# Kernel tuning notes

Hardware: AMD Instinct MI355X
Metric: run time of the kernel (lower is better)

Reference implementation:

```python
import jax, jax.numpy as jnp
import numpy as np

TEMP = 0.07  # softmax temperature T


def _l2norm(x, axis=1, eps=1e-12):
    return x / jnp.clip(jnp.linalg.norm(x, axis=axis, keepdims=True), eps, None)


def setup_inputs() -> dict:
    key = jax.random.key(0)
    k1, k2, k3, k4 = jax.random.split(key, 4)
    B, K, D = 256, 8192, 128
    q = jax.random.normal(k1, (B, D), dtype=jnp.float32)
    ba_queue = _l2norm(jax.random.normal(k2, (K, D), dtype=jnp.float32))
    nonba_queue = _l2norm(jax.random.normal(k3, (K, D), dtype=jnp.float32))
    targets = jax.random.randint(k4, (B,), 0, 2, dtype=jnp.int64)
    return {"q": q, "ba_queue": ba_queue, "nonba_queue": nonba_queue, "targets": targets}


def reference(q, ba_queue, nonba_queue, targets):
    K = ba_queue.shape[0]
    # encoder output is L2-normalized; queues are detached buffers
    qn = _l2norm(q, axis=1)
    all_feature = jnp.concatenate([qn, ba_queue, nonba_queue], axis=0)  # [N, D]
    all_label = jnp.concatenate([
        targets.astype(jnp.int32),
        jnp.ones((K,), dtype=jnp.int32),
        jnp.zeros((K,), dtype=jnp.int32),
    ])  # [N]
    N = all_feature.shape[0]

    # [N, N] similarity logits
    sim = jnp.matmul(all_feature, all_feature.T) / TEMP
    logits = sim - jax.lax.stop_gradient(jnp.max(sim, axis=1, keepdims=True))

    # positive mask (same label), excluding self
    mask = (all_label[:, None] == all_label[None, :]).astype(jnp.float32)
    logits_mask = 1.0 - jnp.eye(N, dtype=jnp.float32)
    mask = mask * logits_mask

    exp_logits = jnp.exp(logits) * logits_mask
    log_prob = logits - jnp.log(jnp.sum(exp_logits, axis=1, keepdims=True))
    mean_log_prob_pos = jnp.sum(mask * log_prob, axis=1) / jnp.sum(mask, axis=1)
    return -jnp.mean(mean_log_prob_pos)
```

## Files before the change

kernel.cpp:

```cpp
#include <hip/hip_runtime.h>
#include <hip/hip_bf16.h>
#include <stdint.h>

#define TEMPERATURE 0.07f
#define SC 20.6099312f

constexpr int NQ = 256;
constexpr int KQ = 8192;
constexpr int D  = 128;
constexpr int N  = NQ + 2 * KQ;
constexpr int CS = 26;
constexpr int CS2 = CS * 2;
constexpr int BN = 128;
constexpr int RBM = N / 128;
constexpr int RBF = N / 256;
constexpr int PB = 520;

typedef float f32x16 __attribute__((ext_vector_type(16)));
typedef int   i32x4  __attribute__((ext_vector_type(4)));
typedef int   i32x8  __attribute__((ext_vector_type(8)));

constexpr size_t OFF_F32  = 0;
constexpr size_t OFF_8    = OFF_F32  + (size_t)NQ * D * 4;
constexpr size_t OFF_8S   = OFF_8    + (size_t)N * D;
constexpr size_t OFF_PART = OFF_8S   + (size_t)N * D;
constexpr size_t OFF_ATOM = OFF_PART + (size_t)CS2 * N * 4;
constexpr size_t ATOM_BYTES = 256 * 8 + 16;

#define MFMA8(a, b, c) __builtin_amdgcn_mfma_scale_f32_32x32x64_f8f6f4( \
    (a), (b), (c), 0, 0, 0, 0x7f7f7f7f, 0, 0x7f7f7f7f)

__global__ __launch_bounds__(256) void k_prep(const float* __restrict__ q,
                                              const float* __restrict__ ba,
                                              const float* __restrict__ nb,
                                              const long long* __restrict__ tgt,
                                              float* __restrict__ ff,
                                              unsigned char* __restrict__ fb8,
                                              unsigned char* __restrict__ fb8s,
                                              unsigned long long* __restrict__ iS) {
    __shared__ float red[4][2][128];
    int wid = threadIdx.x >> 6, lane = threadIdx.x & 63;
    int rbase = blockIdx.x * 32 + wid * 8;
    float s0x = 0.f, s0y = 0.f, s1x = 0.f, s1y = 0.f;
    #pragma unroll
    for (int i = 0; i < 8; ++i) {
        int r = rbase + i;
        const float* src = (r < NQ) ? (q + (size_t)r * D)
                         : (r < NQ + KQ) ? (ba + (size_t)(r - NQ) * D)
                         : (nb + (size_t)(r - NQ - KQ) * D);
        float2 v = *(const float2*)(src + lane * 2);
        float a = v.x, b = v.y;
        int lab;
        if (r < NQ) {
            float ss = a * a + b * b;
            #pragma unroll
            for (int m = 1; m < 64; m <<= 1) ss += __shfl_xor(ss, m);
            float scale = 1.0f / fmaxf(sqrtf(ss), 1e-12f);
            a *= scale; b *= scale;
            lab = (int)tgt[r];
            *(float2*)(ff + (size_t)r * D + lane * 2) = make_float2(a, b);
        } else {
            lab = (r < NQ + KQ) ? 1 : 0;
        }
        int w8  = __builtin_amdgcn_cvt_pk_fp8_f32(a, b, 0, false);
        int w8s = __builtin_amdgcn_cvt_pk_fp8_f32(a * SC, b * SC, 0, false);
        *(unsigned short*)(fb8  + (size_t)r * D + lane * 2) = (unsigned short)w8;
        *(unsigned short*)(fb8s + (size_t)r * D + lane * 2) = (unsigned short)w8s;
        if (lab) { s1x += a; s1y += b; } else { s0x += a; s0y += b; }
    }
    red[wid][0][lane * 2]     = s0x;
    red[wid][0][lane * 2 + 1] = s0y;
    red[wid][1][lane * 2]     = s1x;
    red[wid][1][lane * 2 + 1] = s1y;
    __syncthreads();
    int lab2 = threadIdx.x >> 7, d = threadIdx.x & 127;
    float s = red[0][lab2][d] + red[1][lab2][d] + red[2][lab2][d] + red[3][lab2][d];
    long long fx = __double2ll_rn((double)s * 4294967296.0);
    atomicAdd(&iS[lab2 * 128 + d], (unsigned long long)fx);
}

__global__ __launch_bounds__(256, 4) void k_main(const unsigned char* __restrict__ fb8,
                                                 const unsigned char* __restrict__ fb8s,
                                                 float* __restrict__ part) {
    __shared__ __align__(16) unsigned char lds[2][BN * 128];
    const int bid = blockIdx.x;
    const int rb = bid / CS, cs = bid % CS;
    const int tid = threadIdx.x;
    const int lane = tid & 63;
    const int wid  = tid >> 6;
    const int wr = wid >> 1, wc = wid & 1;
    const int l31 = lane & 31, lhi = lane >> 5;
    const int rw = rb * 128 + wr * 64;

    int soff[4];
    #pragma unroll
    for (int i = 0; i < 4; ++i) {
        int flat = i * 256 + tid;
        int line = flat >> 4, p = flat & 15;
        int pl = p ^ (line & 15);
        soff[i] = (2 * line + (pl >> 3)) * 128 + (pl & 7) * 16;
    }

#define STAGE(T, B) { \
    const unsigned char* base_ = fb8 + ((size_t)(cs + (T) * CS)) * (BN * 128); \
    _Pragma("unroll") \
    for (int i_ = 0; i_ < 4; ++i_) \
        __builtin_amdgcn_global_load_lds( \
            (const __attribute__((address_space(1))) unsigned int*)(base_ + soff[i_]), \
            (__attribute__((address_space(3))) unsigned int*)(&lds[B][(i_ * 256 + tid) * 16]), \
            16, 0, 0); }

#define SYNC() { asm volatile("s_waitcnt vmcnt(0)" ::: "memory"); __builtin_amdgcn_s_barrier(); }

    i32x8 rf[2][2];
    #pragma unroll
    for (int rs = 0; rs < 2; ++rs)
        #pragma unroll
        for (int s = 0; s < 2; ++s)
            rf[rs][s] = *(const i32x8*)(fb8s + (size_t)(rw + rs * 32 + l31) * D + s * 64 + lhi * 32);

    f32x16 z16;
    #pragma unroll
    for (int e = 0; e < 16; ++e) z16[e] = 0.f;

    float2 ps2[2] = {{0.f, 0.f}, {0.f, 0.f}};

    STAGE(0, 0) SYNC()

    #pragma unroll 1
    for (int t = 0; t < 5; ++t) {
        if (t + 1 < 5) STAGE(t + 1, (t & 1) ^ 1)
        const unsigned char* buf = &lds[t & 1][0];

        f32x16 acc[2][2];
        __builtin_amdgcn_s_setprio(1);
        #pragma unroll
        for (int s = 0; s < 2; ++s) {
            #pragma unroll
            for (int cc = 0; cc < 2; ++cc) {
                int crow = wc * 64 + cc * 32 + l31;
                int line = crow >> 1;
                int pb = ((crow & 1) << 3) + s * 4 + lhi * 2;
                const unsigned char* lb = buf + line * 256;
                i32x4 lo = *(const i32x4*)(lb + ((pb    ) ^ (line & 15)) * 16);
                i32x4 hi = *(const i32x4*)(lb + ((pb + 1) ^ (line & 15)) * 16);
                i32x8 a = {lo[0], lo[1], lo[2], lo[3], hi[0], hi[1], hi[2], hi[3]};
                acc[cc][0] = MFMA8(a, rf[0][s], (s == 0) ? z16 : acc[cc][0]);
                acc[cc][1] = MFMA8(a, rf[1][s], (s == 0) ? z16 : acc[cc][1]);
            }
        }
        __builtin_amdgcn_s_setprio(0);

        #pragma unroll
        for (int cc = 0; cc < 2; ++cc)
            #pragma unroll
            for (int rs = 0; rs < 2; ++rs) {
                float2 p = {0.f, 0.f};
                #pragma unroll
                for (int g = 0; g < 8; ++g) {
                    p.x += __builtin_amdgcn_exp2f(acc[cc][rs][2 * g]);
                    p.y += __builtin_amdgcn_exp2f(acc[cc][rs][2 * g + 1]);
                }
                ps2[rs].x += p.x; ps2[rs].y += p.y;
            }

        SYNC()
    }

    float rsum[2] = {ps2[0].x + ps2[0].y, ps2[1].x + ps2[1].y};
    rsum[0] += __shfl_xor(rsum[0], 32);
    rsum[1] += __shfl_xor(rsum[1], 32);
    if (lane < 32) {
        float* dst = part + (size_t)(cs * 2 + wc) * N + rw + lane;
        dst[0]  = rsum[0];
        dst[32] = rsum[1];
    }
#undef STAGE
#undef SYNC
}

__global__ __launch_bounds__(256) void k_rowfin(const float* __restrict__ part,
                                                const float* __restrict__ ff,
                                                const float* __restrict__ ba,
                                                const float* __restrict__ nb,
                                                unsigned long long* __restrict__ atom,
                                                const long long* __restrict__ tgt,
                                                float* __restrict__ out) {
    __shared__ float sS[256];
    __shared__ float red[256];
    __shared__ int scnt[2];
    sS[threadIdx.x] = (float)((double)(long long)atom[threadIdx.x] * (1.0 / 4294967296.0));
    if (threadIdx.x < 64) {
        int c = 0;
        #pragma unroll
        for (int i = 0; i < 4; ++i) c += (int)tgt[threadIdx.x + 64 * i];
        #pragma unroll
        for (int m = 1; m < 64; m <<= 1) c += __shfl_xor(c, m);
        if (threadIdx.x == 0) { scnt[0] = (NQ - c) + KQ; scnt[1] = c + KQ; }
    }
    __syncthreads();
    int r = blockIdx.x * 256 + threadIdx.x;
    float se = 0.f;
    #pragma unroll 4
    for (int c = 0; c < CS2; ++c) se += part[(size_t)c * N + r];
    int lab = (r < NQ) ? (int)tgt[r] : ((r < NQ + KQ) ? 1 : 0);
    const float* fsrc = (r < NQ) ? (ff + (size_t)r * D)
                      : (r < NQ + KQ) ? (ba + (size_t)(r - NQ) * D)
                      : (nb + (size_t)(r - NQ - KQ) * D);
    const float4* frow = (const float4*)fsrc;
    const float4* srow = (const float4*)(sS + lab * 128);
    float dS = 0.f, dd = 0.f;
    #pragma unroll
    for (int i = 0; i < 32; ++i) {
        float4 f = frow[i];
        float4 s = srow[i];
        dS += f.x * s.x + f.y * s.y + f.z * s.z + f.w * s.w;
        int wa  = __builtin_amdgcn_cvt_pk_fp8_f32(f.x, f.y, 0, false);
        int wb  = __builtin_amdgcn_cvt_pk_fp8_f32(f.z, f.w, 0, false);
        int wsa = __builtin_amdgcn_cvt_pk_fp8_f32(f.x * SC, f.y * SC, 0, false);
        int wsb = __builtin_amdgcn_cvt_pk_fp8_f32(f.z * SC, f.w * SC, 0, false);
        dd += __builtin_amdgcn_cvt_f32_fp8(wa, 0) * __builtin_amdgcn_cvt_f32_fp8(wsa, 0)
            + __builtin_amdgcn_cvt_f32_fp8(wa, 1) * __builtin_amdgcn_cvt_f32_fp8(wsa, 1)
            + __builtin_amdgcn_cvt_f32_fp8(wb, 0) * __builtin_amdgcn_cvt_f32_fp8(wsb, 0)
            + __builtin_amdgcn_cvt_f32_fp8(wb, 1) * __builtin_amdgcn_cvt_f32_fp8(wsb, 1);
    }
    se -= __builtin_amdgcn_exp2f(dd);
    float lse = logf(se);
    float P = (float)(scnt[lab] - 1);
    float mlpp = (dS - 1.0f) / (TEMPERATURE * P) - lse;
    red[threadIdx.x] = mlpp;
    __syncthreads();
    for (int s2 = 128; s2 > 0; s2 >>= 1) {
        if (threadIdx.x < s2) red[threadIdx.x] += red[threadIdx.x + s2];
        __syncthreads();
    }
    if (threadIdx.x == 0) {
        unsigned long long* lacc = atom + 256;
        unsigned long long* done = atom + 257;
        long long fx = __double2ll_rn((double)red[0] * 16777216.0);
        atomicAdd(lacc, (unsigned long long)fx);
        __threadfence();
        unsigned long long old = atomicAdd(done, 1ull);
        if (old == (unsigned long long)(RBF - 1)) {
            __threadfence();
            long long tot = (long long)atomicAdd(lacc, 0ull);
            out[0] = (float)(-((double)tot * (1.0 / 16777216.0)) / (double)N);
        }
    }
}

extern "C" void kernel_launch(void* const* d_in, const int* in_sizes, int n_in,
                              void* d_out, int out_size, void* d_ws, size_t ws_size,
                              hipStream_t stream) {
    const float* q       = (const float*)d_in[0];
    const float* ba      = (const float*)d_in[1];
    const float* nb      = (const float*)d_in[2];
    const long long* tgt = (const long long*)d_in[3];
    char* ws = (char*)d_ws;
    float*              ff   = (float*)(ws + OFF_F32);
    unsigned char*      fb8  = (unsigned char*)(ws + OFF_8);
    unsigned char*      fb8s = (unsigned char*)(ws + OFF_8S);
    float*              part = (float*)(ws + OFF_PART);
    unsigned long long* atom = (unsigned long long*)(ws + OFF_ATOM);

    hipMemsetAsync(atom, 0, ATOM_BYTES, stream);
    k_prep  <<<PB,       256, 0, stream>>>(q, ba, nb, tgt, ff, fb8, fb8s, atom);
    k_main  <<<RBM * CS, 256, 0, stream>>>(fb8, fb8s, part);
    k_rowfin<<<RBF,      256, 0, stream>>>(part, ff, ba, nb, atom, tgt, (float*)d_out);
}
```

Baseline: 84.09 us.

## Fuse row finalization into main kernel via last-block-per-row-tile ticket

Removes the separate k_rowfin launch. Each k_main block increments a per-row-block atomic counter, and the last of the CS column-slice blocks for a row tile does the finalization in place: it sums the partials, computes the self term and dot products split across two half-threads per row, then reduces into a global accumulator. This saves a kernel launch and lets finalization overlap with other blocks still doing matmul work. The cost is an extra atomic and fence per block, and finalization now runs on only 128 threads per tile inside a kernel with tight occupancy limits.

```diff
diff --git a/kernel.cpp b/kernel.cpp
--- a/kernel.cpp
+++ b/kernel.cpp
@@ -13,7 +13,6 @@
 constexpr int CS2 = CS * 2;
 constexpr int BN = 128;
 constexpr int RBM = N / 128;
-constexpr int RBF = N / 256;
 constexpr int PB = 520;
 
 typedef float f32x16 __attribute__((ext_vector_type(16)));
@@ -25,7 +24,10 @@
 constexpr size_t OFF_8S   = OFF_8    + (size_t)N * D;
 constexpr size_t OFF_PART = OFF_8S   + (size_t)N * D;
 constexpr size_t OFF_ATOM = OFF_PART + (size_t)CS2 * N * 4;
-constexpr size_t ATOM_BYTES = 256 * 8 + 16;
+constexpr int AT_RBD = 256;
+constexpr int AT_LACC = 390;
+constexpr int AT_DONE2 = 391;
+constexpr size_t ATOM_BYTES = 392 * 8;
 
 #define MFMA8(a, b, c) __builtin_amdgcn_mfma_scale_f32_32x32x64_f8f6f4( \
     (a), (b), (c), 0, 0, 0, 0x7f7f7f7f, 0, 0x7f7f7f7f)
@@ -81,8 +83,15 @@
 
 __global__ __launch_bounds__(256, 4) void k_main(const unsigned char* __restrict__ fb8,
                                                  const unsigned char* __restrict__ fb8s,
-                                                 float* __restrict__ part) {
+                                                 const float* __restrict__ ff,
+                                                 const float* __restrict__ ba,
+                                                 const float* __restrict__ nb,
+                                                 const long long* __restrict__ tgt,
+                                                 float* __restrict__ part,
+                                                 unsigned long long* __restrict__ atom,
+                                                 float* __restrict__ out) {
     __shared__ __align__(16) unsigned char lds[2][BN * 128];
+    __shared__ unsigned long long tick;
     const int bid = blockIdx.x;
     const int rb = bid / CS, cs = bid % CS;
     const int tid = threadIdx.x;
@@ -175,78 +184,97 @@
         dst[0]  = rsum[0];
         dst[32] = rsum[1];
     }
+
+    __syncthreads();
+    if (tid == 0) {
+        __threadfence();
+        tick = atomicAdd(&atom[AT_RBD + rb], 1ull);
+    }
+    __syncthreads();
+    if (tick != (unsigned long long)(CS - 1)) return;
+    __threadfence();
+
+    float* sS  = (float*)&lds[0][0];
+    float* pse = sS + 256;
+    float* pdS = pse + 256;
+    float* pdd = pdS + 256;
+    float* red = pdd + 256;
+    __shared__ int scnt[2];
+
+    sS[tid] = (float)((double)(long long)atom[tid] * (1.0 / 4294967296.0));
+    if (tid < 64) {
+        int c = 0;
+        #pragma unroll
+        for (int i = 0; i < 4; ++i) c += (int)tgt[tid + 64 * i];
+        #pragma unroll
+        for (int m = 1; m < 64; m <<= 1) c += __shfl_xor(c, m);
+        if (tid == 0) { scnt[0] = (NQ - c) + KQ; scnt[1] = c + KQ; }
+    }
+    __syncthreads();
+
+    {
+        int h = tid >> 7, rr = tid & 127;
+        int r = rb * 128 + rr;
+        float se = 0.f;
+        #pragma unroll 2
+        for (int c = h * CS; c < h * CS + CS; ++c) se += part[(size_t)c * N + r];
+        int lab = (r < NQ) ? (int)tgt[r] : ((r < NQ + KQ) ? 1 : 0);
+        const float* fsrc = (r < NQ) ? (ff + (size_t)r * D)
+                          : (r < NQ + KQ) ? (ba + (size_t)(r - NQ) * D)
+                          : (nb + (size_t)(r - NQ - KQ) * D);
+        const float4* frow = (const float4*)(fsrc + h * 64);
+        const float4* srow = (const float4*)(sS + lab * 128 + h * 64);
+        float dS = 0.f, dd = 0.f;
+        #pragma unroll
+        for (int i = 0; i < 16; ++i) {
+            float4 f = frow[i];
+            float4 s = srow[i];
+            dS += f.x * s.x + f.y * s.y + f.z * s.z + f.w * s.w;
+            int wa  = __builtin_amdgcn_cvt_pk_fp8_f32(f.x, f.y, 0, false);
+            int wb  = __builtin_amdgcn_cvt_pk_fp8_f32(f.z, f.w, 0, false);
+            int wsa = __builtin_amdgcn_cvt_pk_fp8_f32(f.x * SC, f.y * SC, 0, false);
+            int wsb = __builtin_amdgcn_cvt_pk_fp8_f32(f.z * SC, f.w * SC, 0, false);
+            dd += __builtin_amdgcn_cvt_f32_fp8(wa, 0) * __builtin_amdgcn_cvt_f32_fp8(wsa, 0)
+                + __builtin_amdgcn_cvt_f32_fp8(wa, 1) * __builtin_amdgcn_cvt_f32_fp8(wsa, 1)
+                + __builtin_amdgcn_cvt_f32_fp8(wb, 0) * __builtin_amdgcn_cvt_f32_fp8(wsb, 0)
+                + __builtin_amdgcn_cvt_f32_fp8(wb, 1) * __builtin_amdgcn_cvt_f32_fp8(wsb, 1);
+        }
+        pse[h * 128 + rr] = se;
+        pdS[h * 128 + rr] = dS;
+        pdd[h * 128 + rr] = dd;
+    }
+    __syncthreads();
+
+    if (tid < 128) {
+        int rr = tid;
+        int r = rb * 128 + rr;
+        float se = pse[rr] + pse[128 + rr];
+        float dS = pdS[rr] + pdS[128 + rr];
+        float dd = pdd[rr] + pdd[128 + rr];
+        se -= __builtin_amdgcn_exp2f(dd);
+        float lse = logf(se);
+        int lab = (r < NQ) ? (int)tgt[r] : ((r < NQ + KQ) ? 1 : 0);
+        float P = (float)(scnt[lab] - 1);
+        red[rr] = (dS - 1.0f) / (TEMPERATURE * P) - lse;
+    }
+    __syncthreads();
+    for (int s2 = 64; s2 > 0; s2 >>= 1) {
+        if (tid < s2) red[tid] += red[tid + s2];
+        __syncthreads();
+    }
+    if (tid == 0) {
+        long long fx = __double2ll_rn((double)red[0] * 16777216.0);
+        atomicAdd(&atom[AT_LACC], (unsigned long long)fx);
+        __threadfence();
+        unsigned long long old = atomicAdd(&atom[AT_DONE2], 1ull);
+        if (old == (unsigned long long)(RBM - 1)) {
+            __threadfence();
+            long long tot = (long long)atomicAdd(&atom[AT_LACC], 0ull);
+            out[0] = (float)(-((double)tot * (1.0 / 16777216.0)) / (double)N);
+        }
+    }
 #undef STAGE
 #undef SYNC
-}
-
-__global__ __launch_bounds__(256) void k_rowfin(const float* __restrict__ part,
-                                                const float* __restrict__ ff,
-                                                const float* __restrict__ ba,
-                                                const float* __restrict__ nb,
-                                                unsigned long long* __restrict__ atom,
-                                                const long long* __restrict__ tgt,
-                                                float* __restrict__ out) {
-    __shared__ float sS[256];
-    __shared__ float red[256];
-    __shared__ int scnt[2];
-    sS[threadIdx.x] = (float)((double)(long long)atom[threadIdx.x] * (1.0 / 4294967296.0));
-    if (threadIdx.x < 64) {
-        int c = 0;
-        #pragma unroll
-        for (int i = 0; i < 4; ++i) c += (int)tgt[threadIdx.x + 64 * i];
-        #pragma unroll
-        for (int m = 1; m < 64; m <<= 1) c += __shfl_xor(c, m);
-        if (threadIdx.x == 0) { scnt[0] = (NQ - c) + KQ; scnt[1] = c + KQ; }
-    }
-    __syncthreads();
-    int r = blockIdx.x * 256 + threadIdx.x;
-    float se = 0.f;
-    #pragma unroll 4
-    for (int c = 0; c < CS2; ++c) se += part[(size_t)c * N + r];
-    int lab = (r < NQ) ? (int)tgt[r] : ((r < NQ + KQ) ? 1 : 0);
-    const float* fsrc = (r < NQ) ? (ff + (size_t)r * D)
-                      : (r < NQ + KQ) ? (ba + (size_t)(r - NQ) * D)
-                      : (nb + (size_t)(r - NQ - KQ) * D);
-    const float4* frow = (const float4*)fsrc;
-    const float4* srow = (const float4*)(sS + lab * 128);
-    float dS = 0.f, dd = 0.f;
-    #pragma unroll
-    for (int i = 0; i < 32; ++i) {
-        float4 f = frow[i];
-        float4 s = srow[i];
-        dS += f.x * s.x + f.y * s.y + f.z * s.z + f.w * s.w;
-        int wa  = __builtin_amdgcn_cvt_pk_fp8_f32(f.x, f.y, 0, false);
-        int wb  = __builtin_amdgcn_cvt_pk_fp8_f32(f.z, f.w, 0, false);
-        int wsa = __builtin_amdgcn_cvt_pk_fp8_f32(f.x * SC, f.y * SC, 0, false);
-        int wsb = __builtin_amdgcn_cvt_pk_fp8_f32(f.z * SC, f.w * SC, 0, false);
-        dd += __builtin_amdgcn_cvt_f32_fp8(wa, 0) * __builtin_amdgcn_cvt_f32_fp8(wsa, 0)
-            + __builtin_amdgcn_cvt_f32_fp8(wa, 1) * __builtin_amdgcn_cvt_f32_fp8(wsa, 1)
-            + __builtin_amdgcn_cvt_f32_fp8(wb, 0) * __builtin_amdgcn_cvt_f32_fp8(wsb, 0)
-            + __builtin_amdgcn_cvt_f32_fp8(wb, 1) * __builtin_amdgcn_cvt_f32_fp8(wsb, 1);
-    }
-    se -= __builtin_amdgcn_exp2f(dd);
-    float lse = logf(se);
-    float P = (float)(scnt[lab] - 1);
-    float mlpp = (dS - 1.0f) / (TEMPERATURE * P) - lse;
-    red[threadIdx.x] = mlpp;
-    __syncthreads();
-    for (int s2 = 128; s2 > 0; s2 >>= 1) {
-        if (threadIdx.x < s2) red[threadIdx.x] += red[threadIdx.x + s2];
-        __syncthreads();
-    }
-    if (threadIdx.x == 0) {
-        unsigned long long* lacc = atom + 256;
-        unsigned long long* done = atom + 257;
-        long long fx = __double2ll_rn((double)red[0] * 16777216.0);
-        atomicAdd(lacc, (unsigned long long)fx);
-        __threadfence();
-        unsigned long long old = atomicAdd(done, 1ull);
-        if (old == (unsigned long long)(RBF - 1)) {
-            __threadfence();
-            long long tot = (long long)atomicAdd(lacc, 0ull);
-            out[0] = (float)(-((double)tot * (1.0 / 16777216.0)) / (double)N);
-        }
-    }
 }
 
 extern "C" void kernel_launch(void* const* d_in, const int* in_sizes, int n_in,
@@ -264,7 +292,7 @@
     unsigned long long* atom = (unsigned long long*)(ws + OFF_ATOM);
 
     hipMemsetAsync(atom, 0, ATOM_BYTES, stream);
-    k_prep  <<<PB,       256, 0, stream>>>(q, ba, nb, tgt, ff, fb8, fb8s, atom);
-    k_main  <<<RBM * CS, 256, 0, stream>>>(fb8, fb8s, part);
-    k_rowfin<<<RBF,      256, 0, stream>>>(part, ff, ba, nb, atom, tgt, (float*)d_out);
+    k_prep<<<PB,       256, 0, stream>>>(q, ba, nb, tgt, ff, fb8, fb8s, atom);
+    k_main<<<RBM * CS, 256, 0, stream>>>(fb8, fb8s, ff, ba, nb, tgt, part, atom,
+                                         (float*)d_out);
 }
```

New measurement: 270.2 us. 3.21x slower.
